# Kernel optimization log

Hardware: AMD Instinct MI355X
Metric: run time of the kernel (lower is better)

## Reference

```python
import jax, jax.numpy as jnp
import numpy as np

H, I, SI, E = 2048, 1408, 5632, 60
B, S = 1, 512


def setup_inputs() -> dict:
    key = jax.random.key(0)
    ks = jax.random.split(key, 9)
    sc = 0.02  # weight init scale for numerical stability
    return {
        "hidden_states": jax.random.normal(ks[0], (B, S, H), dtype=jnp.float32),
        "router_w": jax.random.normal(ks[1], (E, H), dtype=jnp.float32) * sc,
        "gate_w": jax.random.normal(ks[2], (E, I, H), dtype=jnp.float32) * sc,
        "up_w": jax.random.normal(ks[3], (E, I, H), dtype=jnp.float32) * sc,
        "down_w": jax.random.normal(ks[4], (E, H, I), dtype=jnp.float32) * sc,
        "sh_gate_w": jax.random.normal(ks[5], (SI, H), dtype=jnp.float32) * sc,
        "sh_up_w": jax.random.normal(ks[6], (SI, H), dtype=jnp.float32) * sc,
        "sh_down_w": jax.random.normal(ks[7], (H, SI), dtype=jnp.float32) * sc,
        "expert_gate_w": jax.random.normal(ks[8], (1, H), dtype=jnp.float32) * sc,
        "top_k": 4,
    }


NORM_TOPK_PROB = False  # Qwen1.5-MoE config


def reference(hidden_states, router_w, gate_w, up_w, down_w,
              sh_gate_w, sh_up_w, sh_down_w, expert_gate_w, top_k):
    b, s, h = hidden_states.shape
    x = hidden_states.reshape(-1, h)                      # [T, H]

    # --- router: softmax over all experts, then top-k sparse weights ---
    logits = x @ router_w.T                               # [T, E]
    probs = jax.nn.softmax(logits.astype(jnp.float32), axis=-1)
    vals, idx = jax.lax.top_k(probs, top_k)               # [T, k]
    if NORM_TOPK_PROB:
        vals = vals / jnp.sum(vals, axis=-1, keepdims=True)
    # scatter top-k weights back to dense [T, E] (zeros elsewhere)
    onehot = jax.nn.one_hot(idx, E, dtype=probs.dtype)    # [T, k, E]
    w = jnp.einsum('tke,tk->te', onehot, vals).astype(x.dtype)  # [T, E]

    # --- grouped GLU experts (dense-masked faithful reference) ---
    g = jnp.einsum('td,eid->tei', x, gate_w)              # [T, E, I]
    a = jax.nn.silu(g) * jnp.einsum('td,eid->tei', x, up_w)
    moe = jnp.einsum('tei,ehi,te->th', a, down_w, w)      # [T, H]

    # --- shared expert with sigmoid gate ---
    shared = (jax.nn.silu(x @ sh_gate_w.T) * (x @ sh_up_w.T)) @ sh_down_w.T
    shared = jax.nn.sigmoid(x @ expert_gate_w.T) * shared # [T,1]*[T,H]

    return (moe + shared).reshape(b, s, h)
```

## Files before the change

kernel.cpp:

```cpp
#include <hip/hip_runtime.h>
#include <hip/hip_bf16.h>
#include <stdint.h>

#define TOKENS 512
#define HDIM   2048
#define IDIM   1408
#define SIDIM  5632
#define NEXP   60
#define TOPK   4
#define NSLOTS (TOKENS*TOPK)
#define ROWPAD 64

#define VMWAIT(N) asm volatile("s_waitcnt vmcnt(" #N ")" ::: "memory")
#define SBAR()    asm volatile("s_barrier" ::: "memory")

typedef __attribute__((ext_vector_type(8))) short bf16x8;
typedef __attribute__((ext_vector_type(4))) float f32x4;

__device__ __forceinline__ short f2bf(float f){
  uint32_t u = __float_as_uint(f);
  u = (u + 0x7fffu + ((u >> 16) & 1u)) >> 16;
  return (short)(u & 0xffffu);
}

__device__ __forceinline__ bf16x8 pack8(float4 a, float4 b){
  bf16x8 r;
  r[0]=f2bf(a.x); r[1]=f2bf(a.y); r[2]=f2bf(a.z); r[3]=f2bf(a.w);
  r[4]=f2bf(b.x); r[5]=f2bf(b.y); r[6]=f2bf(b.z); r[7]=f2bf(b.w);
  return r;
}

__device__ __forceinline__ bf16x8 as_bf16x8(float4 v){
  union { float4 f; bf16x8 b; } u; u.f = v; return u.b;
}

__device__ __forceinline__ f32x4 zero4(){
  f32x4 z; z[0]=0.f; z[1]=0.f; z[2]=0.f; z[3]=0.f; return z;
}

__device__ __forceinline__ f32x4 mfma16(bf16x8 a, bf16x8 b, f32x4 c){
  return __builtin_amdgcn_mfma_f32_16x16x32_bf16(a, b, c, 0, 0, 0);
}

__device__ __forceinline__ void stage_w32(float4* tile, const float* __restrict__ W,
                                          int K, int k0, int tid){
  int l = tid & 63, wv = tid >> 6;
  #pragma unroll
  for (int j=0;j<2;j++){
    int u0 = j*256 + wv*64;
    int u  = u0 + l;
    int row = u >> 3;
    int lu  = ((u & 7) - (row & 7)) & 7;
    const float* src = W + (size_t)row*K + k0 + lu*4;
    __builtin_amdgcn_global_load_lds(
        (const __attribute__((address_space(1))) void*)src,
        (__attribute__((address_space(3))) void*)(tile + u0), 16, 0, 0);
  }
}

__device__ __forceinline__ bf16x8 read_wfrag32(const float4* tile, int r, int kq){
  int rot = r & 7;
  const float4* row = tile + (size_t)r*8;
  float4 f0 = row[(2*kq     + rot) & 7];
  float4 f1 = row[(2*kq + 1 + rot) & 7];
  return pack8(f0, f1);
}

__device__ __forceinline__ void stage_a32(float4* tile, const short* __restrict__ Arows,
                                          int K, int k0, int tid){
  int l = tid & 63, wv = tid >> 6;
  int u0 = wv*64;
  int u  = u0 + l;
  int row = u >> 2;
  int lu  = ((u & 3) - (row & 3)) & 3;
  const short* src = Arows + (size_t)row*K + k0 + lu*8;
  __builtin_amdgcn_global_load_lds(
      (const __attribute__((address_space(1))) void*)src,
      (__attribute__((address_space(3))) void*)(tile + u0), 16, 0, 0);
}

__device__ __forceinline__ void read_afrag32(const float4* tile, int c16, int kq,
                                             bf16x8* av){
  #pragma unroll
  for (int mf=0; mf<4; mf++){
    int row = c16 + 16*mf;
    av[mf] = as_bf16x8(tile[(size_t)row*4 + ((kq + row) & 3)]);
  }
}

__global__ __launch_bounds__(64) void router_kernel(
    const float* __restrict__ x, const float* __restrict__ rw,
    const float* __restrict__ egw, int* __restrict__ topk_idx,
    float* __restrict__ topk_w, float* __restrict__ gates,
    int* __restrict__ counts)
{
  int t = blockIdx.x;
  int lane = threadIdx.x;
  const float* xr = x + (size_t)t*HDIM;
  float xv[HDIM/64];
  #pragma unroll
  for (int i=0;i<HDIM/64;i++) xv[i] = xr[lane + 64*i];

  float mylogit = -1e30f;
  for (int e=0;e<NEXP;e++){
    const float* w = rw + (size_t)e*HDIM;
    float acc = 0.f;
    #pragma unroll
    for (int i=0;i<HDIM/64;i++) acc += xv[i]*w[lane+64*i];
    #pragma unroll
    for (int s=32;s>0;s>>=1) acc += __shfl_xor(acc, s);
    if (lane == e) mylogit = acc;
  }
  {
    float acc = 0.f;
    #pragma unroll
    for (int i=0;i<HDIM/64;i++) acc += xv[i]*egw[lane+64*i];
    #pragma unroll
    for (int s=32;s>0;s>>=1) acc += __shfl_xor(acc, s);
    if (lane == 0) gates[t] = 1.f/(1.f + __expf(-acc));
  }
  float m = mylogit;
  #pragma unroll
  for (int s=32;s>0;s>>=1) m = fmaxf(m, __shfl_xor(m, s));
  float p = (lane < NEXP) ? __expf(mylogit - m) : 0.f;
  float sum = p;
  #pragma unroll
  for (int s=32;s>0;s>>=1) sum += __shfl_xor(sum, s);
  float prob = p / sum;
  for (int k=0;k<TOPK;k++){
    float v = prob; int idx = lane;
    #pragma unroll
    for (int s=32;s>0;s>>=1){
      float ov = __shfl_xor(v, s); int oi = __shfl_xor(idx, s);
      if (ov > v || (ov == v && oi < idx)){ v = ov; idx = oi; }
    }
    if (lane == 0){
      topk_idx[t*TOPK+k] = idx;
      topk_w[t*TOPK+k]  = v;
      atomicAdd(&counts[idx], 1);
    }
    if (lane == idx) prob = -1e30f;
  }
}

__global__ __launch_bounds__(256) void scatter_kernel(
    const float* __restrict__ x, const int* __restrict__ topk_idx,
    const int* __restrict__ counts, int* __restrict__ offsets,
    int* __restrict__ fill, int* __restrict__ slot_of,
    __hip_bfloat16* __restrict__ xg, __hip_bfloat16* __restrict__ xb)
{
  int t = blockIdx.x, tid = threadIdx.x;
  if (tid == 0){
    int e0 = topk_idx[t*TOPK+0], e1 = topk_idx[t*TOPK+1];
    int e2 = topk_idx[t*TOPK+2], e3 = topk_idx[t*TOPK+3];
    int o0=0,o1=0,o2=0,o3=0, acc=0;
    for (int e=0;e<NEXP;e++){
      int c = counts[e];
      if (t == 0) offsets[e] = acc;
      if (e==e0) o0=acc; if (e==e1) o1=acc;
      if (e==e2) o2=acc; if (e==e3) o3=acc;
      acc += c;
    }
    if (t == 0) offsets[NEXP] = acc;
    slot_of[t*TOPK+0] = o0 + atomicAdd(&fill[e0],1);
    slot_of[t*TOPK+1] = o1 + atomicAdd(&fill[e1],1);
    slot_of[t*TOPK+2] = o2 + atomicAdd(&fill[e2],1);
    slot_of[t*TOPK+3] = o3 + atomicAdd(&fill[e3],1);
  }
  __syncthreads();
  int4 sl = ((const int4*)slot_of)[t];
  const float4* xr = (const float4*)(x + (size_t)t*HDIM);
  float4 v0 = xr[tid*2], v1 = xr[tid*2+1];
  bf16x8 b = pack8(v0, v1);
  *(bf16x8*)((short*)xb + (size_t)t*HDIM + tid*8) = b;
  *(bf16x8*)((short*)xg + (size_t)sl.x*HDIM + tid*8) = b;
  *(bf16x8*)((short*)xg + (size_t)sl.y*HDIM + tid*8) = b;
  *(bf16x8*)((short*)xg + (size_t)sl.z*HDIM + tid*8) = b;
  *(bf16x8*)((short*)xg + (size_t)sl.w*HDIM + tid*8) = b;
}

__global__ __launch_bounds__(256, 4) void gateup_all(
    const float* __restrict__ gW_e, const float* __restrict__ uW_e,
    const __hip_bfloat16* __restrict__ A_e, __hip_bfloat16* __restrict__ out_e,
    const float* __restrict__ gW_s, const float* __restrict__ uW_s,
    const __hip_bfloat16* __restrict__ A_s, __hip_bfloat16* __restrict__ out_s,
    const int* __restrict__ offsets)
{
  extern __shared__ __align__(16) char smem[];
  float4* G0 = (float4*)smem;
  float4* G1 = G0 + 512;
  float4* U0 = G1 + 512;
  float4* U1 = U0 + 512;
  float4* A0 = U1 + 512;
  float4* A1 = A0 + 256;

  int bid = blockIdx.x;
  int xcd = bid & 7, pos = bid >> 3;
  const float *Wg, *Wu; const short *Abase; short *outp;
  int NI, bx, m_start, m_end;
  if (pos < 88){
    bx = pos;
    Wg = gW_s; Wu = uW_s; Abase = (const short*)A_s; outp = (short*)out_s;
    NI = SIDIM;
    m_start = xcd*64; m_end = m_start + 64;
  } else {
    int q = xcd*165 + (pos - 88);
    int e = q/22; bx = q - e*22;
    size_t wo = (size_t)e * IDIM * HDIM;
    Wg = gW_e + wo; Wu = uW_e + wo;
    Abase = (const short*)A_e; outp = (short*)out_e;
    NI = IDIM;
    m_start = offsets[e]; m_end = offsets[e+1];
  }
  if (m_start >= m_end) return;
  const int K = HDIM;

  int tid  = threadIdx.x;
  int lane = tid & 63;
  int wv   = tid >> 6;
  int c16 = lane & 15, kq = lane >> 4;
  int wrow = bx*64 + wv*16 + c16;
  int r    = wv*16 + c16;
  const float* WgT = Wg + (size_t)(bx*64)*K;
  const float* WuT = Wu + (size_t)(bx*64)*K;

  for (int m0 = m_start; m0 < m_end; m0 += 64){
    int mrem = m_end - m0;
    const short* Ar = Abase + (size_t)m0*K;
    f32x4 accg[4], accu[4];
    #pragma unroll
    for (int i=0;i<4;i++){ accg[i] = zero4(); accu[i] = zero4(); }

    stage_w32(G0, WgT, K, 0, tid);
    stage_w32(U0, WuT, K, 0, tid);
    stage_a32(A0, Ar,  K, 0, tid);

    for (int k0 = 0; k0 < K; k0 += 64){
      stage_w32(G1, WgT, K, k0+32, tid);
      stage_w32(U1, WuT, K, k0+32, tid);
      stage_a32(A1, Ar,  K, k0+32, tid);
      VMWAIT(5); SBAR();
      {
        bf16x8 av[4];
        read_afrag32(A0, c16, kq, av);
        bf16x8 bg = read_wfrag32(G0, r, kq);
        bf16x8 bu = read_wfrag32(U0, r, kq);
        #pragma unroll
        for (int mf=0; mf<4; mf++){
          accg[mf] = mfma16(av[mf], bg, accg[mf]);
          accu[mf] = mfma16(av[mf], bu, accu[mf]);
        }
      }
      SBAR();
      if (k0 + 64 < K){
        stage_w32(G0, WgT, K, k0+64, tid);
        stage_w32(U0, WuT, K, k0+64, tid);
        stage_a32(A0, Ar,  K, k0+64, tid);
        VMWAIT(5);
      } else {
        VMWAIT(0);
      }
      SBAR();
      {
        bf16x8 av[4];
        read_afrag32(A1, c16, kq, av);
        bf16x8 bg = read_wfrag32(G1, r, kq);
        bf16x8 bu = read_wfrag32(U1, r, kq);
        #pragma unroll
        for (int mf=0; mf<4; mf++){
          accg[mf] = mfma16(av[mf], bg, accg[mf]);
          accu[mf] = mfma16(av[mf], bu, accu[mf]);
        }
      }
      SBAR();
    }

    #pragma unroll
    for (int mf=0; mf<4; mf++){
      #pragma unroll
      for (int j=0;j<4;j++){
        int mrow = mf*16 + kq*4 + j;
        if (mrow < mrem){
          float g = accg[mf][j], u = accu[mf][j];
          float s = g * u / (1.f + __expf(-g));
          outp[(size_t)(m0+mrow)*NI + wrow] = f2bf(s);
        }
      }
    }
  }
}

__global__ __launch_bounds__(256, 4) void down_all(
    const float* __restrict__ W_e, const __hip_bfloat16* __restrict__ A_e,
    float* __restrict__ out_e,
    const float* __restrict__ W_s, const __hip_bfloat16* __restrict__ A_s,
    float* __restrict__ out_s,
    const int* __restrict__ offsets)
{
  extern __shared__ __align__(16) char smem[];
  float4* Wb = (float4*)smem;
  float4* Ab = Wb + 3*512;

  int bid = blockIdx.x;
  int xcd = bid & 7, pos = bid >> 3;
  const float* W; const short* Abase; float* outp;
  int K, bx, m_start, m_end;
  if (pos < 32){
    bx = pos;
    W = W_s; Abase = (const short*)A_s; outp = out_s; K = SIDIM;
    m_start = xcd*64; m_end = m_start + 64;
  } else {
    int q = xcd*240 + (pos - 32);
    int e = q >> 5; bx = q & 31;
    W = W_e + (size_t)e * HDIM * IDIM;
    Abase = (const short*)A_e; outp = out_e; K = IDIM;
    m_start = offsets[e]; m_end = offsets[e+1];
  }
  if (m_start >= m_end) return;

  int tid  = threadIdx.x;
  int lane = tid & 63;
  int wv   = tid >> 6;
  int c16 = lane & 15, kq = lane >> 4;
  int wrow = bx*64 + wv*16 + c16;
  int r    = wv*16 + c16;
  const float* WT = W + (size_t)(bx*64)*K;
  int np = K >> 5;

  for (int m0 = m_start; m0 < m_end; m0 += 64){
    int mrem = m_end - m0;
    const short* Ar = Abase + (size_t)m0*K;
    f32x4 acc[4];
    #pragma unroll
    for (int i=0;i<4;i++) acc[i] = zero4();

    stage_w32(Wb,       WT, K, 0,  tid);
    stage_a32(Ab,       Ar, K, 0,  tid);
    stage_w32(Wb + 512, WT, K, 32, tid);
    stage_a32(Ab + 256, Ar, K, 32, tid);

    int cs = 0, ss = 2;
    for (int p = 0; p < np; ++p){
      if (p + 2 < np){
        stage_w32(Wb + ss*512, WT, K, (p+2) << 5, tid);
        stage_a32(Ab + ss*256, Ar, K, (p+2) << 5, tid);
        VMWAIT(6);
      } else if (p + 1 < np){
        VMWAIT(3);
      } else {
        VMWAIT(0);
      }
      SBAR();
      {
        bf16x8 av[4];
        read_afrag32(Ab + cs*256, c16, kq, av);
        bf16x8 b = read_wfrag32(Wb + cs*512, r, kq);
        #pragma unroll
        for (int mf=0; mf<4; mf++)
          acc[mf] = mfma16(av[mf], b, acc[mf]);
      }
      SBAR();
      cs = (cs == 2) ? 0 : cs + 1;
      ss = (ss == 2) ? 0 : ss + 1;
    }

    #pragma unroll
    for (int mf=0; mf<4; mf++){
      #pragma unroll
      for (int j=0;j<4;j++){
        int mrow = mf*16 + kq*4 + j;
        if (mrow < mrem)
          outp[(size_t)(m0+mrow)*HDIM + wrow] = acc[mf][j];
      }
    }
  }
}

__global__ __launch_bounds__(256) void combine_kernel(
    const float* __restrict__ dslot, const float* __restrict__ shdown,
    const int* __restrict__ slot_of, const float* __restrict__ topw,
    const float* __restrict__ gates, float* __restrict__ out)
{
  int t = blockIdx.x, tid = threadIdx.x;
  int4  sl = ((const int4*)slot_of)[t];
  float4 w = ((const float4*)topw)[t];
  float sg = gates[t];
  const float* r0 = dslot + (size_t)sl.x*HDIM;
  const float* r1 = dslot + (size_t)sl.y*HDIM;
  const float* r2 = dslot + (size_t)sl.z*HDIM;
  const float* r3 = dslot + (size_t)sl.w*HDIM;
  const float* rs = shdown + (size_t)t*HDIM;
  float* o = out + (size_t)t*HDIM;
  #pragma unroll
  for (int it=0; it<HDIM/(256*4); ++it){
    int h = (tid + it*256) * 4;
    float4 a0 = *(const float4*)(r0+h);
    float4 a1 = *(const float4*)(r1+h);
    float4 a2 = *(const float4*)(r2+h);
    float4 a3 = *(const float4*)(r3+h);
    float4 as = *(const float4*)(rs+h);
    float4 r;
    r.x = w.x*a0.x + w.y*a1.x + w.z*a2.x + w.w*a3.x + sg*as.x;
    r.y = w.x*a0.y + w.y*a1.y + w.z*a2.y + w.w*a3.y + sg*as.y;
    r.z = w.x*a0.z + w.y*a1.z + w.z*a2.z + w.w*a3.z + sg*as.z;
    r.w = w.x*a0.w + w.y*a1.w + w.z*a2.w + w.w*a3.w + sg*as.w;
    *(float4*)(o+h) = r;
  }
}

extern "C" void kernel_launch(void* const* d_in, const int* in_sizes, int n_in,
                              void* d_out, int out_size, void* d_ws, size_t ws_size,
                              hipStream_t stream)
{
  const float* x         = (const float*)d_in[0];
  const float* router_w  = (const float*)d_in[1];
  const float* gate_w    = (const float*)d_in[2];
  const float* up_w      = (const float*)d_in[3];
  const float* down_w    = (const float*)d_in[4];
  const float* sh_gate_w = (const float*)d_in[5];
  const float* sh_up_w   = (const float*)d_in[6];
  const float* sh_down_w = (const float*)d_in[7];
  const float* eg_w      = (const float*)d_in[8];

  char* p = (char*)d_ws;
  auto alloc = [&](size_t bytes)->char*{
    char* r = p; p += (bytes + 255) & ~(size_t)255; return r;
  };
  int*   counts   = (int*)  alloc(NEXP*4);
  int*   fill     = (int*)  alloc(NEXP*4);
  int*   offsets  = (int*)  alloc((NEXP+1)*4);
  int*   topk_idx = (int*)  alloc(NSLOTS*4);
  float* topk_w   = (float*)alloc(NSLOTS*4);
  int*   slot_of  = (int*)  alloc(NSLOTS*4);
  float* gates    = (float*)alloc(TOKENS*4);
  __hip_bfloat16* xb    = (__hip_bfloat16*)alloc((size_t)TOKENS*HDIM*2);
  __hip_bfloat16* xg    = (__hip_bfloat16*)alloc((size_t)(NSLOTS+ROWPAD)*HDIM*2);
  __hip_bfloat16* act   = (__hip_bfloat16*)alloc((size_t)(NSLOTS+ROWPAD)*IDIM*2);
  __hip_bfloat16* shact = (__hip_bfloat16*)alloc((size_t)TOKENS*SIDIM*2);
  float* dslot  = (float*)alloc((size_t)NSLOTS*HDIM*4);
  float* shdown = (float*)alloc((size_t)TOKENS*HDIM*4);
  if ((size_t)(p - (char*)d_ws) > ws_size) return;

  hipMemsetAsync(counts, 0, NEXP*4, stream);
  hipMemsetAsync(fill,   0, NEXP*4, stream);

  router_kernel <<<TOKENS, 64, 0, stream>>>(x, router_w, eg_w, topk_idx, topk_w, gates, counts);
  scatter_kernel<<<TOKENS, 256, 0, stream>>>(x, topk_idx, counts, offsets, fill, slot_of, xg, xb);

  gateup_all<<<2024, 256, 40*1024, stream>>>(
      gate_w, up_w, xg, act,
      sh_gate_w, sh_up_w, xb, shact, offsets);

  down_all<<<2176, 256, 36*1024, stream>>>(
      down_w, act, dslot,
      sh_down_w, shact, shdown, offsets);

  combine_kernel<<<TOKENS, 256, 0, stream>>>(dslot, shdown, slot_of, topk_w, gates, (float*)d_out);
}
```

Before: 647.7 us.

## Enlarge shared-expert gate/up tiles to 256 tokens to reuse weight loads

In the fused gate/up kernel, shared-expert blocks now each cover 256 token rows (four 64-row sub-tiles) instead of 64, so every fp32 weight tile is staged once per half of the tokens rather than once per 64-token chunk. This cuts the redundant global weight traffic for the large shared-expert matrices, and the grid shrinks to match. In exchange, accumulator register use and LDS per block rise (64KB, launch bounds lowered to 2 blocks per SIMD), which reduces occupancy and latency hiding.

Result: faster. 595.8 us (-8.0%).

```diff
diff --git a/kernel.cpp b/kernel.cpp
--- a/kernel.cpp
+++ b/kernel.cpp
@@ -179,7 +179,7 @@
   *(bf16x8*)((short*)xg + (size_t)sl.w*HDIM + tid*8) = b;
 }
 
-__global__ __launch_bounds__(256, 4) void gateup_all(
+__global__ __launch_bounds__(256, 2) void gateup_all(
     const float* __restrict__ gW_e, const float* __restrict__ uW_e,
     const __hip_bfloat16* __restrict__ A_e, __hip_bfloat16* __restrict__ out_e,
     const float* __restrict__ gW_s, const float* __restrict__ uW_s,
@@ -187,103 +187,194 @@
     const int* __restrict__ offsets)
 {
   extern __shared__ __align__(16) char smem[];
-  float4* G0 = (float4*)smem;
-  float4* G1 = G0 + 512;
-  float4* U0 = G1 + 512;
-  float4* U1 = U0 + 512;
-  float4* A0 = U1 + 512;
-  float4* A1 = A0 + 256;
-
   int bid = blockIdx.x;
   int xcd = bid & 7, pos = bid >> 3;
-  const float *Wg, *Wu; const short *Abase; short *outp;
-  int NI, bx, m_start, m_end;
-  if (pos < 88){
-    bx = pos;
-    Wg = gW_s; Wu = uW_s; Abase = (const short*)A_s; outp = (short*)out_s;
-    NI = SIDIM;
-    m_start = xcd*64; m_end = m_start + 64;
-  } else {
-    int q = xcd*165 + (pos - 88);
-    int e = q/22; bx = q - e*22;
-    size_t wo = (size_t)e * IDIM * HDIM;
-    Wg = gW_e + wo; Wu = uW_e + wo;
-    Abase = (const short*)A_e; outp = (short*)out_e;
-    NI = IDIM;
-    m_start = offsets[e]; m_end = offsets[e+1];
-  }
-  if (m_start >= m_end) return;
-  const int K = HDIM;
-
   int tid  = threadIdx.x;
   int lane = tid & 63;
   int wv   = tid >> 6;
   int c16 = lane & 15, kq = lane >> 4;
-  int wrow = bx*64 + wv*16 + c16;
-  int r    = wv*16 + c16;
-  const float* WgT = Wg + (size_t)(bx*64)*K;
-  const float* WuT = Wu + (size_t)(bx*64)*K;
-
-  for (int m0 = m_start; m0 < m_end; m0 += 64){
-    int mrem = m_end - m0;
-    const short* Ar = Abase + (size_t)m0*K;
-    f32x4 accg[4], accu[4];
-    #pragma unroll
-    for (int i=0;i<4;i++){ accg[i] = zero4(); accu[i] = zero4(); }
+  const int K = HDIM;
+
+  if (pos < 22){
+    float4* G0 = (float4*)smem;
+    float4* G1 = G0 + 512;
+    float4* U0 = G1 + 512;
+    float4* U1 = U0 + 512;
+    float4* A0 = U1 + 512;
+    float4* A1 = A0 + 1024;
+
+    int s  = xcd*22 + pos;
+    int bx = s % 88;
+    int half = s / 88;
+    int wrow = bx*64 + wv*16 + c16;
+    int r    = wv*16 + c16;
+    const float* WgT = gW_s + (size_t)(bx*64)*K;
+    const float* WuT = uW_s + (size_t)(bx*64)*K;
+    const short* Ab0 = (const short*)A_s + (size_t)(half*256)*K;
+    short* outp = (short*)out_s;
+
+    f32x4 accg[4][4], accu[4][4];
+    #pragma unroll
+    for (int mt=0; mt<4; mt++)
+      #pragma unroll
+      for (int i=0;i<4;i++){ accg[mt][i] = zero4(); accu[mt][i] = zero4(); }
 
     stage_w32(G0, WgT, K, 0, tid);
     stage_w32(U0, WuT, K, 0, tid);
-    stage_a32(A0, Ar,  K, 0, tid);
+    #pragma unroll
+    for (int mt=0; mt<4; mt++)
+      stage_a32(A0 + mt*256, Ab0 + (size_t)mt*64*K, K, 0, tid);
 
     for (int k0 = 0; k0 < K; k0 += 64){
       stage_w32(G1, WgT, K, k0+32, tid);
       stage_w32(U1, WuT, K, k0+32, tid);
-      stage_a32(A1, Ar,  K, k0+32, tid);
-      VMWAIT(5); SBAR();
+      #pragma unroll
+      for (int mt=0; mt<4; mt++)
+        stage_a32(A1 + mt*256, Ab0 + (size_t)mt*64*K, K, k0+32, tid);
+      VMWAIT(8); SBAR();
       {
-        bf16x8 av[4];
-        read_afrag32(A0, c16, kq, av);
         bf16x8 bg = read_wfrag32(G0, r, kq);
         bf16x8 bu = read_wfrag32(U0, r, kq);
         #pragma unroll
-        for (int mf=0; mf<4; mf++){
-          accg[mf] = mfma16(av[mf], bg, accg[mf]);
-          accu[mf] = mfma16(av[mf], bu, accu[mf]);
+        for (int mt=0; mt<4; mt++){
+          bf16x8 av[4];
+          read_afrag32(A0 + mt*256, c16, kq, av);
+          #pragma unroll
+          for (int mf=0; mf<4; mf++){
+            accg[mt][mf] = mfma16(av[mf], bg, accg[mt][mf]);
+            accu[mt][mf] = mfma16(av[mf], bu, accu[mt][mf]);
+          }
         }
       }
       SBAR();
       if (k0 + 64 < K){
         stage_w32(G0, WgT, K, k0+64, tid);
         stage_w32(U0, WuT, K, k0+64, tid);
-        stage_a32(A0, Ar,  K, k0+64, tid);
-        VMWAIT(5);
+        #pragma unroll
+        for (int mt=0; mt<4; mt++)
+          stage_a32(A0 + mt*256, Ab0 + (size_t)mt*64*K, K, k0+64, tid);
+        VMWAIT(8);
       } else {
         VMWAIT(0);
       }
       SBAR();
       {
-        bf16x8 av[4];
-        read_afrag32(A1, c16, kq, av);
         bf16x8 bg = read_wfrag32(G1, r, kq);
         bf16x8 bu = read_wfrag32(U1, r, kq);
         #pragma unroll
-        for (int mf=0; mf<4; mf++){
-          accg[mf] = mfma16(av[mf], bg, accg[mf]);
-          accu[mf] = mfma16(av[mf], bu, accu[mf]);
+        for (int mt=0; mt<4; mt++){
+          bf16x8 av[4];
+          read_afrag32(A1 + mt*256, c16, kq, av);
+          #pragma unroll
+          for (int mf=0; mf<4; mf++){
+            accg[mt][mf] = mfma16(av[mf], bg, accg[mt][mf]);
+            accu[mt][mf] = mfma16(av[mf], bu, accu[mt][mf]);
+          }
         }
       }
       SBAR();
     }
 
     #pragma unroll
-    for (int mf=0; mf<4; mf++){
+    for (int mt=0; mt<4; mt++){
       #pragma unroll
-      for (int j=0;j<4;j++){
-        int mrow = mf*16 + kq*4 + j;
-        if (mrow < mrem){
-          float g = accg[mf][j], u = accu[mf][j];
-          float s = g * u / (1.f + __expf(-g));
-          outp[(size_t)(m0+mrow)*NI + wrow] = f2bf(s);
+      for (int mf=0; mf<4; mf++){
+        #pragma unroll
+        for (int j=0;j<4;j++){
+          int row = half*256 + mt*64 + mf*16 + kq*4 + j;
+          float g = accg[mt][mf][j], u = accu[mt][mf][j];
+          float sv = g * u / (1.f + __expf(-g));
+          outp[(size_t)row*SIDIM + wrow] = f2bf(sv);
+        }
+      }
+    }
+    return;
+  }
+
+  {
+    float4* G0 = (float4*)smem;
+    float4* G1 = G0 + 512;
+    float4* U0 = G1 + 512;
+    float4* U1 = U0 + 512;
+    float4* A0 = U1 + 512;
+    float4* A1 = A0 + 256;
+
+    int q = xcd*165 + (pos - 22);
+    int e = q/22, bx = q - e*22;
+    size_t wo = (size_t)e * IDIM * HDIM;
+    const float* Wg = gW_e + wo;
+    const float* Wu = uW_e + wo;
+    const short* Abase = (const short*)A_e;
+    short* outp = (short*)out_e;
+    int m_start = offsets[e], m_end = offsets[e+1];
+    if (m_start >= m_end) return;
+
+    int wrow = bx*64 + wv*16 + c16;
+    int r    = wv*16 + c16;
+    const float* WgT = Wg + (size_t)(bx*64)*K;
+    const float* WuT = Wu + (size_t)(bx*64)*K;
+
+    for (int m0 = m_start; m0 < m_end; m0 += 64){
+      int mrem = m_end - m0;
+      const short* Ar = Abase + (size_t)m0*K;
+      f32x4 accg[4], accu[4];
+      #pragma unroll
+      for (int i=0;i<4;i++){ accg[i] = zero4(); accu[i] = zero4(); }
+
+      stage_w32(G0, WgT, K, 0, tid);
+      stage_w32(U0, WuT, K, 0, tid);
+      stage_a32(A0, Ar,  K, 0, tid);
+
+      for (int k0 = 0; k0 < K; k0 += 64){
+        stage_w32(G1, WgT, K, k0+32, tid);
+        stage_w32(U1, WuT, K, k0+32, tid);
+        stage_a32(A1, Ar,  K, k0+32, tid);
+        VMWAIT(5); SBAR();
+        {
+          bf16x8 av[4];
+          read_afrag32(A0, c16, kq, av);
+          bf16x8 bg = read_wfrag32(G0, r, kq);
+          bf16x8 bu = read_wfrag32(U0, r, kq);
+          #pragma unroll
+          for (int mf=0; mf<4; mf++){
+            accg[mf] = mfma16(av[mf], bg, accg[mf]);
+            accu[mf] = mfma16(av[mf], bu, accu[mf]);
+          }
+        }
+        SBAR();
+        if (k0 + 64 < K){
+          stage_w32(G0, WgT, K, k0+64, tid);
+          stage_w32(U0, WuT, K, k0+64, tid);
+          stage_a32(A0, Ar,  K, k0+64, tid);
+          VMWAIT(5);
+        } else {
+          VMWAIT(0);
+        }
+        SBAR();
+        {
+          bf16x8 av[4];
+          read_afrag32(A1, c16, kq, av);
+          bf16x8 bg = read_wfrag32(G1, r, kq);
+          bf16x8 bu = read_wfrag32(U1, r, kq);
+          #pragma unroll
+          for (int mf=0; mf<4; mf++){
+            accg[mf] = mfma16(av[mf], bg, accg[mf]);
+            accu[mf] = mfma16(av[mf], bu, accu[mf]);
+          }
+        }
+        SBAR();
+      }
+
+      #pragma unroll
+      for (int mf=0; mf<4; mf++){
+        #pragma unroll
+        for (int j=0;j<4;j++){
+          int mrow = mf*16 + kq*4 + j;
+          if (mrow < mrem){
+            float g = accg[mf][j], u = accu[mf][j];
+            float sv = g * u / (1.f + __expf(-g));
+            outp[(size_t)(m0+mrow)*IDIM + wrow] = f2bf(sv);
+          }
         }
       }
     }
@@ -447,7 +538,7 @@
   router_kernel <<<TOKENS, 64, 0, stream>>>(x, router_w, eg_w, topk_idx, topk_w, gates, counts);
   scatter_kernel<<<TOKENS, 256, 0, stream>>>(x, topk_idx, counts, offsets, fill, slot_of, xg, xb);
 
-  gateup_all<<<2024, 256, 40*1024, stream>>>(
+  gateup_all<<<1496, 256, 64*1024, stream>>>(
       gate_w, up_w, xg, act,
       sh_gate_w, sh_up_w, xb, shact, offsets);
 
```
